# Kernel tuning notes

Measured on AMD Instinct MI355X. Metric: run time of the kernel, lower is better.

## Reference

```python
import jax, jax.numpy as jnp
import numpy as np

B, T, D, DO = 8, 2048, 1024, 1024

def setup_inputs() -> dict:
    key = jax.random.key(0)
    ks = jax.random.split(key, 7)
    s = 1.0 / np.sqrt(D)
    return {
        "input_tensor": jax.random.normal(ks[0], (B, T, D), dtype=jnp.float32),
        "Wq": jax.random.uniform(ks[1], (D, D), jnp.float32, -s, s),
        "bq": jax.random.uniform(ks[2], (D,), jnp.float32, -s, s),
        "Wk": jax.random.uniform(ks[3], (D, D), jnp.float32, -s, s),
        "bk": jax.random.uniform(ks[4], (D,), jnp.float32, -s, s),
        "Wv": jax.random.uniform(ks[5], (D, DO), jnp.float32, -s, s),
        "bv": jax.random.uniform(ks[6], (DO,), jnp.float32, -s, s),
    }

def reference(input_tensor, Wq, bq, Wk, bk, Wv, bv):
    scale = jnp.sqrt(jnp.float32(input_tensor.shape[-1]))
    q = input_tensor @ Wq + bq            # [B,T,D]
    k = input_tensor @ Wk + bk            # [B,T,D]
    v = input_tensor @ Wv + bv            # [B,T,DO]
    scores = jnp.einsum('btd,bsd->bts', q, k) / scale  # [B,T,T]
    attn = jax.nn.softmax(scores, axis=-1)
    return jnp.einsum('bts,bso->bto', attn, v)         # [B,T,DO]
```

## Files before the change

kernel.cpp:

```cpp
#include <hip/hip_runtime.h>
#include <stdint.h>

typedef unsigned short u16;
typedef __attribute__((ext_vector_type(4))) float    floatx4;
typedef __attribute__((ext_vector_type(8))) __bf16   bf16x8;
typedef __attribute__((ext_vector_type(2))) unsigned int uintx2;
typedef __attribute__((ext_vector_type(4))) unsigned int uintx4;

__device__ inline u16 f2bf(float f) {
  unsigned int u = __builtin_bit_cast(unsigned int, f);
  u += 0x7fffu + ((u >> 16) & 1u);
  return (u16)(u >> 16);
}

#define GLD16(gsrc, ldst)                                                        \
  __builtin_amdgcn_global_load_lds(                                              \
      (__attribute__((address_space(1))) void*)(gsrc),                           \
      (__attribute__((address_space(3))) void*)(ldst), 16, 0, 0)

#define SB() __builtin_amdgcn_sched_barrier(0)

__global__ __launch_bounds__(256) void prep_kernel(const float* __restrict__ x,
                                                   const float* __restrict__ Wq,
                                                   const float* __restrict__ Wk,
                                                   const float* __restrict__ Wv,
                                                   u16* __restrict__ xb,
                                                   u16* __restrict__ WT) {
  const int z = blockIdx.z;
  const int tid = threadIdx.y * 32 + threadIdx.x;
  if (z >= 3) {
    long blk = (long)(z - 3) * 1024 + blockIdx.y * 32 + blockIdx.x;
    long i = (blk * 256 + tid) * 8;
    floatx4 a = *(const floatx4*)(x + i);
    floatx4 b = *(const floatx4*)(x + i + 4);
    uintx4 o;
    o[0] = (unsigned)f2bf(a[0]) | ((unsigned)f2bf(a[1]) << 16);
    o[1] = (unsigned)f2bf(a[2]) | ((unsigned)f2bf(a[3]) << 16);
    o[2] = (unsigned)f2bf(b[0]) | ((unsigned)f2bf(b[1]) << 16);
    o[3] = (unsigned)f2bf(b[2]) | ((unsigned)f2bf(b[3]) << 16);
    *(uintx4*)(xb + i) = o;
    return;
  }
  __shared__ float tile[32][33];
  const float* W = (z == 0) ? Wq : (z == 1) ? Wk : Wv;
  u16* dst = WT + (long)z * 1024 * 1024;
  int bx = blockIdx.x * 32, by = blockIdx.y * 32;
  int tx = threadIdx.x, ty = threadIdx.y;
  for (int i = 0; i < 32; i += 8)
    tile[ty + i][tx] = W[(long)(by + ty + i) * 1024 + bx + tx];
  __syncthreads();
  for (int i = 0; i < 32; i += 8)
    dst[(long)(bx + ty + i) * 1024 + by + tx] = f2bf(tile[tx][ty + i]);
}

#define BM 256
#define BN 256
#define BK 64

template <int MODE, int GN>
__global__ __launch_bounds__(512, 2)
void gemm_bt(const u16* __restrict__ Aall, const u16* __restrict__ Ball,
             void* __restrict__ Call, void* __restrict__ C2,
             const float* __restrict__ bias, const float* __restrict__ bias2,
             float* __restrict__ lsum,
             int M, int N, int K, long aStride, long bStride, long cStride) {
  __shared__ __align__(16) u16 As[2][BM * BK];
  __shared__ __align__(16) u16 Bs[2][BN * BK];

  const int z = blockIdx.z;
  const u16* A  = Aall + (long)z * aStride;
  const u16* Bt = Ball + (long)z * bStride;

  int m_idx, n_idx;
  {
    const int tiles_n = gridDim.x, tiles_m = gridDim.y;
    int nwg = tiles_n * tiles_m;
    int bid = blockIdx.y * tiles_n + blockIdx.x;
    int qq = nwg >> 3;
    int L = (bid & 7) * qq + (bid >> 3);
    int per_group = GN * tiles_m;
    int g = L / per_group;
    int rem = L - g * per_group;
    n_idx = g * GN + rem % GN;
    m_idx = rem / GN;
  }

  const int tid  = threadIdx.x;
  const int m0   = m_idx * BM;
  const int n0   = n_idx * BN;
  const int wave = tid >> 6;
  const int lane = tid & 63;
  const int wm   = (wave >> 2) * 128;
  const int wn   = (wave & 3) * 64;
  const int l15  = lane & 15;
  const int quad = lane >> 4;

  floatx4 acc[8][4];
  floatx4 zero = {0.f, 0.f, 0.f, 0.f};
#pragma unroll
  for (int i = 0; i < 8; ++i)
#pragma unroll
    for (int j = 0; j < 4; ++j) acc[i][j] = zero;

  const int swz   = (quad ^ (l15 & 7)) * 8;
  const int aOff0 = (wm + l15) * 64 + swz;
  const int bOff0 = (wn + l15) * 64 + swz;

  const u16* gA[4];
  const u16* gB[4];
#pragma unroll
  for (int i = 0; i < 4; ++i) {
    int ci = i * 512 + tid;
    int r = ci >> 3, sc = ci & 7;
    int col = (sc ^ (r & 7)) * 8;
    gA[i] = A  + (long)(m0 + r) * K + col;
    gB[i] = Bt + (long)(n0 + r) * K + col;
  }

  const int nt = K / BK;

  {
    u16* lA = (u16*)As + tid * 8;
    u16* lB = (u16*)Bs + tid * 8;
    GLD16(gB[0], lB);          GLD16(gB[1], lB + 4096);
    GLD16(gB[2], lB + 8192);   GLD16(gB[3], lB + 12288);
    GLD16(gA[0], lA);          GLD16(gA[2], lA + 8192);
    GLD16(gA[1], lA + 4096);   GLD16(gA[3], lA + 12288);
  }
  SB();
  asm volatile("s_waitcnt vmcnt(0)" ::: "memory");
  SB();
  __builtin_amdgcn_s_barrier();
  SB();
#pragma unroll
  for (int i = 0; i < 4; ++i) { gA[i] += BK; gB[i] += BK; }

  for (int t = 0; t < nt; ++t) {
    const int cur = t & 1;
    const int bo  = cur << 14;
    const u16* aP0 = (const u16*)As + bo + aOff0;
    const u16* bP0 = (const u16*)Bs + bo + bOff0;
    const u16* aP1 = (const u16*)As + bo + (aOff0 ^ 32);
    const u16* bP1 = (const u16*)Bs + bo + (bOff0 ^ 32);
    u16* ldsAn = (u16*)As + (bo ^ 16384) + tid * 8;
    u16* ldsBn = (u16*)Bs + (bo ^ 16384) + tid * 8;
    const bool st1 = (t + 1 < nt);
    bf16x8 afA[4], afB[4], bfr[4];

#pragma unroll
    for (int mi = 0; mi < 4; ++mi)
      afA[mi] = *(const bf16x8*)(aP0 + mi * 1024);
#pragma unroll
    for (int ni = 0; ni < 4; ++ni)
      bfr[ni] = *(const bf16x8*)(bP0 + ni * 1024);
    if (st1) { GLD16(gB[0], ldsBn); GLD16(gB[1], ldsBn + 4096); }
    SB();
    if (st1) asm volatile("s_waitcnt vmcnt(2)" ::: "memory");
    else     asm volatile("s_waitcnt vmcnt(0)" ::: "memory");
    SB();
    __builtin_amdgcn_s_barrier();
    asm volatile("s_waitcnt lgkmcnt(0)" ::: "memory");
    SB();
    __builtin_amdgcn_s_setprio(1);
#pragma unroll
    for (int mi = 0; mi < 4; ++mi)
#pragma unroll
      for (int ni = 0; ni < 4; ++ni)
        acc[mi][ni] = __builtin_amdgcn_mfma_f32_16x16x32_bf16(
            bfr[ni], afA[mi], acc[mi][ni], 0, 0, 0);
    __builtin_amdgcn_s_setprio(0);
    SB();

#pragma unroll
    for (int mi = 0; mi < 4; ++mi)
      afB[mi] = *(const bf16x8*)(aP0 + 4096 + mi * 1024);
    if (st1) { GLD16(gB[2], ldsBn + 8192); GLD16(gB[3], ldsBn + 12288); }
    SB();
    __builtin_amdgcn_s_barrier();
    asm volatile("s_waitcnt lgkmcnt(0)" ::: "memory");
    SB();
    __builtin_amdgcn_s_setprio(1);
#pragma unroll
    for (int mi = 0; mi < 4; ++mi)
#pragma unroll
      for (int ni = 0; ni < 4; ++ni)
        acc[4 + mi][ni] = __builtin_amdgcn_mfma_f32_16x16x32_bf16(
            bfr[ni], afB[mi], acc[4 + mi][ni], 0, 0, 0);
    __builtin_amdgcn_s_setprio(0);
    SB();

#pragma unroll
    for (int mi = 0; mi < 4; ++mi)
      afA[mi] = *(const bf16x8*)(aP1 + mi * 1024);
#pragma unroll
    for (int ni = 0; ni < 4; ++ni)
      bfr[ni] = *(const bf16x8*)(bP1 + ni * 1024);
    if (st1) { GLD16(gA[0], ldsAn); GLD16(gA[2], ldsAn + 8192); }
    SB();
    __builtin_amdgcn_s_barrier();
    asm volatile("s_waitcnt lgkmcnt(0)" ::: "memory");
    SB();
    __builtin_amdgcn_s_setprio(1);
#pragma unroll
    for (int mi = 0; mi < 4; ++mi)
#pragma unroll
      for (int ni = 0; ni < 4; ++ni)
        acc[mi][ni] = __builtin_amdgcn_mfma_f32_16x16x32_bf16(
            bfr[ni], afA[mi], acc[mi][ni], 0, 0, 0);
    __builtin_amdgcn_s_setprio(0);
    SB();

#pragma unroll
    for (int mi = 0; mi < 4; ++mi)
      afB[mi] = *(const bf16x8*)(aP1 + 4096 + mi * 1024);
    if (st1) { GLD16(gA[1], ldsAn + 4096); GLD16(gA[3], ldsAn + 12288); }
    SB();
    if (st1) asm volatile("s_waitcnt vmcnt(2)" ::: "memory");
    SB();
    __builtin_amdgcn_s_barrier();
    asm volatile("s_waitcnt lgkmcnt(0)" ::: "memory");
    SB();
    __builtin_amdgcn_s_setprio(1);
#pragma unroll
    for (int mi = 0; mi < 4; ++mi)
#pragma unroll
      for (int ni = 0; ni < 4; ++ni)
        acc[4 + mi][ni] = __builtin_amdgcn_mfma_f32_16x16x32_bf16(
            bfr[ni], afB[mi], acc[4 + mi][ni], 0, 0, 0);
    __builtin_amdgcn_s_setprio(0);
    SB();

#pragma unroll
    for (int i = 0; i < 4; ++i) { gA[i] += BK; gB[i] += BK; }
  }

#pragma unroll
  for (int mi = 0; mi < 8; ++mi) {
    const int row = m0 + wm + mi * 16 + l15;
    if (MODE == 2) {
      u16* C = (u16*)Call + (long)z * cStride;
      float rs = 0.f;
#pragma unroll
      for (int ni = 0; ni < 4; ++ni) {
        int colb = n0 + wn + ni * 16 + quad * 4;
        floatx4 v = acc[mi][ni];
        float e0 = __expf(v[0] * 0.03125f), e1 = __expf(v[1] * 0.03125f);
        float e2 = __expf(v[2] * 0.03125f), e3 = __expf(v[3] * 0.03125f);
        rs += (e0 + e1) + (e2 + e3);
        uintx2 o;
        o[0] = (unsigned)f2bf(e0) | ((unsigned)f2bf(e1) << 16);
        o[1] = (unsigned)f2bf(e2) | ((unsigned)f2bf(e3) << 16);
        *(uintx2*)(C + (long)row * N + colb) = o;
      }
      rs += __shfl_xor(rs, 16);
      rs += __shfl_xor(rs, 32);
      if (quad == 0) atomicAdd(lsum + (long)z * 2048 + row, rs);
    } else if (MODE == 3) {
      float* C = (float*)Call + (long)z * cStride;
      float inv = 1.0f / lsum[(long)z * 2048 + row];
#pragma unroll
      for (int ni = 0; ni < 4; ++ni) {
        int colb = n0 + wn + ni * 16 + quad * 4;
        floatx4 v = acc[mi][ni];
        floatx4 o = {v[0] * inv, v[1] * inv, v[2] * inv, v[3] * inv};
        *(floatx4*)(C + (long)row * N + colb) = o;
      }
    } else if (MODE == 0) {
#pragma unroll
      for (int ni = 0; ni < 4; ++ni) {
        int colb = n0 + wn + ni * 16 + quad * 4;
        u16* C = (colb < 1024) ? (u16*)Call : (u16*)C2;
        const float* bp = (colb < 1024) ? bias + colb : bias2 + (colb - 1024);
        floatx4 b = *(const floatx4*)bp;
        floatx4 v = acc[mi][ni];
        uintx2 o;
        o[0] = (unsigned)f2bf(v[0] + b[0]) | ((unsigned)f2bf(v[1] + b[1]) << 16);
        o[1] = (unsigned)f2bf(v[2] + b[2]) | ((unsigned)f2bf(v[3] + b[3]) << 16);
        *(uintx2*)(C + (long)row * 1024 + (colb & 1023)) = o;
      }
    } else {
      u16* C = (u16*)Call;
      float b = bias[row];
#pragma unroll
      for (int ni = 0; ni < 4; ++ni) {
        int colb = n0 + wn + ni * 16 + quad * 4;
        long base = ((long)(colb >> 11) * 1024) * 2048 + (colb & 2047);
        floatx4 v = acc[mi][ni];
        uintx2 o;
        o[0] = (unsigned)f2bf(v[0] + b) | ((unsigned)f2bf(v[1] + b) << 16);
        o[1] = (unsigned)f2bf(v[2] + b) | ((unsigned)f2bf(v[3] + b) << 16);
        *(uintx2*)(C + base + (long)row * 2048) = o;
      }
    }
  }
}

extern "C" void kernel_launch(void* const* d_in, const int* in_sizes, int n_in,
                              void* d_out, int out_size, void* d_ws, size_t ws_size,
                              hipStream_t stream) {
  const float* x  = (const float*)d_in[0];
  const float* Wq = (const float*)d_in[1];
  const float* bq = (const float*)d_in[2];
  const float* Wk = (const float*)d_in[3];
  const float* bk = (const float*)d_in[4];
  const float* Wv = (const float*)d_in[5];
  const float* bv = (const float*)d_in[6];
  float* out = (float*)d_out;

  const long BT = 16384;
  u16* xb = (u16*)d_ws;
  u16* WT = xb + BT * 1024;
  u16* qb = WT + 3L * 1024 * 1024;
  u16* kb = qb + BT * 1024;
  u16* vT = kb + BT * 1024;
  u16* S  = vT + BT * 1024;
  float* lsum = (float*)(S + 8L * 2048 * 2048);

  hipMemsetAsync(lsum, 0, 8 * 2048 * sizeof(float), stream);

  prep_kernel<<<dim3(32, 32, 11), dim3(32, 8), 0, stream>>>(x, Wq, Wk, Wv, xb, WT);

  gemm_bt<0, 8><<<dim3(8, 64, 1), 512, 0, stream>>>(
      xb, WT, qb, kb, bq, bk, nullptr, 16384, 2048, 1024, 0, 0, 0);
  gemm_bt<1, 8><<<dim3(64, 4, 1), 512, 0, stream>>>(
      WT + 2L * 1024 * 1024, xb, vT, nullptr, bv, nullptr, nullptr,
      1024, 16384, 1024, 0, 0, 0);
  gemm_bt<2, 8><<<dim3(8, 8, 8), 512, 0, stream>>>(
      qb, kb, S, nullptr, nullptr, nullptr, lsum,
      2048, 2048, 1024, 2048L * 1024, 2048L * 1024, 2048L * 2048);
  gemm_bt<3, 4><<<dim3(4, 8, 8), 512, 0, stream>>>(
      S, vT, out, nullptr, nullptr, nullptr, lsum,
      2048, 1024, 2048, 2048L * 2048, 1024L * 2048, 2048L * 1024);
}
```

Before: 392.1 us.

## Shrink GEMM tiles to 128x128 and simplify the double-buffered pipeline

Reduces the block tile from 256x256 to 128x128 and raises the occupancy hint to 4 blocks per CU. The K-loop is restructured from four interleaved sub-phases with staggered global loads to two phases, each issuing all next-tile loads at once followed by a full vmcnt(0) wait. Grids are scaled up to match. This trades per-block data reuse and overlap for more blocks and better load balance across CUs, at the risk of more memory traffic and less latency hiding.

```diff
diff --git a/kernel.cpp b/kernel.cpp
--- a/kernel.cpp
+++ b/kernel.cpp
@@ -53,12 +53,12 @@
     dst[(long)(bx + ty + i) * 1024 + by + tx] = f2bf(tile[tx][ty + i]);
 }
 
-#define BM 256
-#define BN 256
+#define BM 128
+#define BN 128
 #define BK 64
 
 template <int MODE, int GN>
-__global__ __launch_bounds__(512, 2)
+__global__ __launch_bounds__(512, 4)
 void gemm_bt(const u16* __restrict__ Aall, const u16* __restrict__ Ball,
              void* __restrict__ Call, void* __restrict__ C2,
              const float* __restrict__ bias, const float* __restrict__ bias2,
@@ -90,26 +90,26 @@
   const int n0   = n_idx * BN;
   const int wave = tid >> 6;
   const int lane = tid & 63;
-  const int wm   = (wave >> 2) * 128;
-  const int wn   = (wave & 3) * 64;
+  const int wm   = (wave >> 2) * 64;
+  const int wn   = (wave & 3) * 32;
   const int l15  = lane & 15;
   const int quad = lane >> 4;
 
-  floatx4 acc[8][4];
+  floatx4 acc[4][2];
   floatx4 zero = {0.f, 0.f, 0.f, 0.f};
 #pragma unroll
-  for (int i = 0; i < 8; ++i)
-#pragma unroll
-    for (int j = 0; j < 4; ++j) acc[i][j] = zero;
+  for (int i = 0; i < 4; ++i)
+#pragma unroll
+    for (int j = 0; j < 2; ++j) acc[i][j] = zero;
 
   const int swz   = (quad ^ (l15 & 7)) * 8;
   const int aOff0 = (wm + l15) * 64 + swz;
   const int bOff0 = (wn + l15) * 64 + swz;
 
-  const u16* gA[4];
-  const u16* gB[4];
-#pragma unroll
-  for (int i = 0; i < 4; ++i) {
+  const u16* gA[2];
+  const u16* gB[2];
+#pragma unroll
+  for (int i = 0; i < 2; ++i) {
     int ci = i * 512 + tid;
     int r = ci >> 3, sc = ci & 7;
     int col = (sc ^ (r & 7)) * 8;
@@ -122,10 +122,8 @@
   {
     u16* lA = (u16*)As + tid * 8;
     u16* lB = (u16*)Bs + tid * 8;
-    GLD16(gB[0], lB);          GLD16(gB[1], lB + 4096);
-    GLD16(gB[2], lB + 8192);   GLD16(gB[3], lB + 12288);
-    GLD16(gA[0], lA);          GLD16(gA[2], lA + 8192);
-    GLD16(gA[1], lA + 4096);   GLD16(gA[3], lA + 12288);
+    GLD16(gA[0], lA); GLD16(gA[1], lA + 4096);
+    GLD16(gB[0], lB); GLD16(gB[1], lB + 4096);
   }
   SB();
   asm volatile("s_waitcnt vmcnt(0)" ::: "memory");
@@ -133,30 +131,30 @@
   __builtin_amdgcn_s_barrier();
   SB();
 #pragma unroll
-  for (int i = 0; i < 4; ++i) { gA[i] += BK; gB[i] += BK; }
+  for (int i = 0; i < 2; ++i) { gA[i] += BK; gB[i] += BK; }
 
   for (int t = 0; t < nt; ++t) {
     const int cur = t & 1;
-    const int bo  = cur << 14;
+    const int bo  = cur << 13;
     const u16* aP0 = (const u16*)As + bo + aOff0;
     const u16* bP0 = (const u16*)Bs + bo + bOff0;
     const u16* aP1 = (const u16*)As + bo + (aOff0 ^ 32);
     const u16* bP1 = (const u16*)Bs + bo + (bOff0 ^ 32);
-    u16* ldsAn = (u16*)As + (bo ^ 16384) + tid * 8;
-    u16* ldsBn = (u16*)Bs + (bo ^ 16384) + tid * 8;
+    u16* ldsAn = (u16*)As + (bo ^ 8192) + tid * 8;
+    u16* ldsBn = (u16*)Bs + (bo ^ 8192) + tid * 8;
     const bool st1 = (t + 1 < nt);
-    bf16x8 afA[4], afB[4], bfr[4];
-
-#pragma unroll
-    for (int mi = 0; mi < 4; ++mi)
-      afA[mi] = *(const bf16x8*)(aP0 + mi * 1024);
-#pragma unroll
-    for (int ni = 0; ni < 4; ++ni)
+    bf16x8 af[4], bfr[2];
+
+#pragma unroll
+    for (int mi = 0; mi < 4; ++mi)
+      af[mi] = *(const bf16x8*)(aP0 + mi * 1024);
+#pragma unroll
+    for (int ni = 0; ni < 2; ++ni)
       bfr[ni] = *(const bf16x8*)(bP0 + ni * 1024);
-    if (st1) { GLD16(gB[0], ldsBn); GLD16(gB[1], ldsBn + 4096); }
-    SB();
-    if (st1) asm volatile("s_waitcnt vmcnt(2)" ::: "memory");
-    else     asm volatile("s_waitcnt vmcnt(0)" ::: "memory");
+    if (st1) {
+      GLD16(gA[0], ldsAn); GLD16(gA[1], ldsAn + 4096);
+      GLD16(gB[0], ldsBn); GLD16(gB[1], ldsBn + 4096);
+    }
     SB();
     __builtin_amdgcn_s_barrier();
     asm volatile("s_waitcnt lgkmcnt(0)" ::: "memory");
@@ -165,16 +163,20 @@
 #pragma unroll
     for (int mi = 0; mi < 4; ++mi)
 #pragma unroll
-      for (int ni = 0; ni < 4; ++ni)
+      for (int ni = 0; ni < 2; ++ni)
         acc[mi][ni] = __builtin_amdgcn_mfma_f32_16x16x32_bf16(
-            bfr[ni], afA[mi], acc[mi][ni], 0, 0, 0);
+            bfr[ni], af[mi], acc[mi][ni], 0, 0, 0);
     __builtin_amdgcn_s_setprio(0);
     SB();
 
 #pragma unroll
     for (int mi = 0; mi < 4; ++mi)
-      afB[mi] = *(const bf16x8*)(aP0 + 4096 + mi * 1024);
-    if (st1) { GLD16(gB[2], ldsBn + 8192); GLD16(gB[3], ldsBn + 12288); }
+      af[mi] = *(const bf16x8*)(aP1 + mi * 1024);
+#pragma unroll
+    for (int ni = 0; ni < 2; ++ni)
+      bfr[ni] = *(const bf16x8*)(bP1 + ni * 1024);
+    SB();
+    asm volatile("s_waitcnt vmcnt(0)" ::: "memory");
     SB();
     __builtin_amdgcn_s_barrier();
     asm volatile("s_waitcnt lgkmcnt(0)" ::: "memory");
@@ -183,65 +185,24 @@
 #pragma unroll
     for (int mi = 0; mi < 4; ++mi)
 #pragma unroll
-      for (int ni = 0; ni < 4; ++ni)
-        acc[4 + mi][ni] = __builtin_amdgcn_mfma_f32_16x16x32_bf16(
-            bfr[ni], afB[mi], acc[4 + mi][ni], 0, 0, 0);
+      for (int ni = 0; ni < 2; ++ni)
+        acc[mi][ni] = __builtin_amdgcn_mfma_f32_16x16x32_bf16(
+            bfr[ni], af[mi], acc[mi][ni], 0, 0, 0);
     __builtin_amdgcn_s_setprio(0);
     SB();
 
 #pragma unroll
-    for (int mi = 0; mi < 4; ++mi)
-      afA[mi] = *(const bf16x8*)(aP1 + mi * 1024);
-#pragma unroll
-    for (int ni = 0; ni < 4; ++ni)
-      bfr[ni] = *(const bf16x8*)(bP1 + ni * 1024);
-    if (st1) { GLD16(gA[0], ldsAn); GLD16(gA[2], ldsAn + 8192); }
-    SB();
-    __builtin_amdgcn_s_barrier();
-    asm volatile("s_waitcnt lgkmcnt(0)" ::: "memory");
-    SB();
-    __builtin_amdgcn_s_setprio(1);
-#pragma unroll
-    for (int mi = 0; mi < 4; ++mi)
-#pragma unroll
-      for (int ni = 0; ni < 4; ++ni)
-        acc[mi][ni] = __builtin_amdgcn_mfma_f32_16x16x32_bf16(
-            bfr[ni], afA[mi], acc[mi][ni], 0, 0, 0);
-    __builtin_amdgcn_s_setprio(0);
-    SB();
-
-#pragma unroll
-    for (int mi = 0; mi < 4; ++mi)
-      afB[mi] = *(const bf16x8*)(aP1 + 4096 + mi * 1024);
-    if (st1) { GLD16(gA[1], ldsAn + 4096); GLD16(gA[3], ldsAn + 12288); }
-    SB();
-    if (st1) asm volatile("s_waitcnt vmcnt(2)" ::: "memory");
-    SB();
-    __builtin_amdgcn_s_barrier();
-    asm volatile("s_waitcnt lgkmcnt(0)" ::: "memory");
-    SB();
-    __builtin_amdgcn_s_setprio(1);
-#pragma unroll
-    for (int mi = 0; mi < 4; ++mi)
-#pragma unroll
-      for (int ni = 0; ni < 4; ++ni)
-        acc[4 + mi][ni] = __builtin_amdgcn_mfma_f32_16x16x32_bf16(
-            bfr[ni], afB[mi], acc[4 + mi][ni], 0, 0, 0);
-    __builtin_amdgcn_s_setprio(0);
-    SB();
-
-#pragma unroll
-    for (int i = 0; i < 4; ++i) { gA[i] += BK; gB[i] += BK; }
-  }
-
-#pragma unroll
-  for (int mi = 0; mi < 8; ++mi) {
+    for (int i = 0; i < 2; ++i) { gA[i] += BK; gB[i] += BK; }
+  }
+
+#pragma unroll
+  for (int mi = 0; mi < 4; ++mi) {
     const int row = m0 + wm + mi * 16 + l15;
     if (MODE == 2) {
       u16* C = (u16*)Call + (long)z * cStride;
       float rs = 0.f;
 #pragma unroll
-      for (int ni = 0; ni < 4; ++ni) {
+      for (int ni = 0; ni < 2; ++ni) {
         int colb = n0 + wn + ni * 16 + quad * 4;
         floatx4 v = acc[mi][ni];
         float e0 = __expf(v[0] * 0.03125f), e1 = __expf(v[1] * 0.03125f);
@@ -259,7 +220,7 @@
       float* C = (float*)Call + (long)z * cStride;
       float inv = 1.0f / lsum[(long)z * 2048 + row];
 #pragma unroll
-      for (int ni = 0; ni < 4; ++ni) {
+      for (int ni = 0; ni < 2; ++ni) {
         int colb = n0 + wn + ni * 16 + quad * 4;
         floatx4 v = acc[mi][ni];
         floatx4 o = {v[0] * inv, v[1] * inv, v[2] * inv, v[3] * inv};
@@ -267,7 +228,7 @@
       }
     } else if (MODE == 0) {
 #pragma unroll
-      for (int ni = 0; ni < 4; ++ni) {
+      for (int ni = 0; ni < 2; ++ni) {
         int colb = n0 + wn + ni * 16 + quad * 4;
         u16* C = (colb < 1024) ? (u16*)Call : (u16*)C2;
         const float* bp = (colb < 1024) ? bias + colb : bias2 + (colb - 1024);
@@ -282,7 +243,7 @@
       u16* C = (u16*)Call;
       float b = bias[row];
 #pragma unroll
-      for (int ni = 0; ni < 4; ++ni) {
+      for (int ni = 0; ni < 2; ++ni) {
         int colb = n0 + wn + ni * 16 + quad * 4;
         long base = ((long)(colb >> 11) * 1024) * 2048 + (colb & 2047);
         floatx4 v = acc[mi][ni];
@@ -320,15 +281,15 @@
 
   prep_kernel<<<dim3(32, 32, 11), dim3(32, 8), 0, stream>>>(x, Wq, Wk, Wv, xb, WT);
 
-  gemm_bt<0, 8><<<dim3(8, 64, 1), 512, 0, stream>>>(
+  gemm_bt<0, 8><<<dim3(16, 128, 1), 512, 0, stream>>>(
       xb, WT, qb, kb, bq, bk, nullptr, 16384, 2048, 1024, 0, 0, 0);
-  gemm_bt<1, 8><<<dim3(64, 4, 1), 512, 0, stream>>>(
+  gemm_bt<1, 8><<<dim3(128, 8, 1), 512, 0, stream>>>(
       WT + 2L * 1024 * 1024, xb, vT, nullptr, bv, nullptr, nullptr,
       1024, 16384, 1024, 0, 0, 0);
-  gemm_bt<2, 8><<<dim3(8, 8, 8), 512, 0, stream>>>(
+  gemm_bt<2, 8><<<dim3(16, 16, 8), 512, 0, stream>>>(
       qb, kb, S, nullptr, nullptr, nullptr, lsum,
       2048, 2048, 1024, 2048L * 1024, 2048L * 1024, 2048L * 2048);
-  gemm_bt<3, 4><<<dim3(4, 8, 8), 512, 0, stream>>>(
+  gemm_bt<3, 4><<<dim3(8, 16, 8), 512, 0, stream>>>(
       S, vT, out, nullptr, nullptr, nullptr, lsum,
       2048, 1024, 2048, 2048L * 2048, 1024L * 2048, 2048L * 1024);
 }
```

New measurement: 424.3 us. 8.2% more time.

## Restructure GEMM main loop into four M-quarter phases covering both K halves

Applied to the files above, without the earlier changes.

Reorganizes the per-tile MFMA schedule so B fragments for both K halves are loaded once up front. Each of four phases then loads two A fragments per K half and runs 16 MFMAs on a quarter of the M accumulators. The global-to-LDS prefetch issue and the vmcnt waits are redistributed across the four phases, and extra barriers are added after each phase. The aim is to shorten per-phase LDS read latency and spread the async copies more evenly, at the cost of more barriers and more live B registers.

```diff
diff --git a/kernel.cpp b/kernel.cpp
--- a/kernel.cpp
+++ b/kernel.cpp
@@ -124,8 +124,8 @@
     u16* lB = (u16*)Bs + tid * 8;
     GLD16(gB[0], lB);          GLD16(gB[1], lB + 4096);
     GLD16(gB[2], lB + 8192);   GLD16(gB[3], lB + 12288);
-    GLD16(gA[0], lA);          GLD16(gA[2], lA + 8192);
-    GLD16(gA[1], lA + 4096);   GLD16(gA[3], lA + 12288);
+    GLD16(gA[0], lA);          GLD16(gA[1], lA + 4096);
+    GLD16(gA[2], lA + 8192);   GLD16(gA[3], lA + 12288);
   }
   SB();
   asm volatile("s_waitcnt vmcnt(0)" ::: "memory");
@@ -145,89 +145,131 @@
     u16* ldsAn = (u16*)As + (bo ^ 16384) + tid * 8;
     u16* ldsBn = (u16*)Bs + (bo ^ 16384) + tid * 8;
     const bool st1 = (t + 1 < nt);
-    bf16x8 afA[4], afB[4], bfr[4];
-
-#pragma unroll
-    for (int mi = 0; mi < 4; ++mi)
-      afA[mi] = *(const bf16x8*)(aP0 + mi * 1024);
-#pragma unroll
-    for (int ni = 0; ni < 4; ++ni)
-      bfr[ni] = *(const bf16x8*)(bP0 + ni * 1024);
+    bf16x8 bfr0[4], bfr1[4];
+    bf16x8 af0[2], af1[2];
+
+#pragma unroll
+    for (int j = 0; j < 2; ++j) {
+      af0[j] = *(const bf16x8*)(aP0 + j * 1024);
+      af1[j] = *(const bf16x8*)(aP1 + j * 1024);
+    }
+#pragma unroll
+    for (int ni = 0; ni < 4; ++ni) {
+      bfr0[ni] = *(const bf16x8*)(bP0 + ni * 1024);
+      bfr1[ni] = *(const bf16x8*)(bP1 + ni * 1024);
+    }
     if (st1) { GLD16(gB[0], ldsBn); GLD16(gB[1], ldsBn + 4096); }
     SB();
+    asm volatile("s_waitcnt lgkmcnt(8)" ::: "memory");
+    SB();
+    __builtin_amdgcn_s_barrier();
+    asm volatile("s_waitcnt lgkmcnt(0)" ::: "memory");
+    SB();
+    __builtin_amdgcn_s_setprio(1);
+#pragma unroll
+    for (int j = 0; j < 2; ++j)
+#pragma unroll
+      for (int ni = 0; ni < 4; ++ni)
+        acc[j][ni] = __builtin_amdgcn_mfma_f32_16x16x32_bf16(
+            bfr0[ni], af0[j], acc[j][ni], 0, 0, 0);
+#pragma unroll
+    for (int j = 0; j < 2; ++j)
+#pragma unroll
+      for (int ni = 0; ni < 4; ++ni)
+        acc[j][ni] = __builtin_amdgcn_mfma_f32_16x16x32_bf16(
+            bfr1[ni], af1[j], acc[j][ni], 0, 0, 0);
+    __builtin_amdgcn_s_setprio(0);
+    SB();
+    __builtin_amdgcn_s_barrier();
+    SB();
+
+#pragma unroll
+    for (int j = 0; j < 2; ++j) {
+      af0[j] = *(const bf16x8*)(aP0 + (2 + j) * 1024);
+      af1[j] = *(const bf16x8*)(aP1 + (2 + j) * 1024);
+    }
+    if (st1) { GLD16(gB[2], ldsBn + 8192); GLD16(gB[3], ldsBn + 12288); }
+    SB();
+    if (st1) asm volatile("s_waitcnt vmcnt(4)" ::: "memory");
+    else     asm volatile("s_waitcnt vmcnt(0)" ::: "memory");
+    SB();
+    __builtin_amdgcn_s_barrier();
+    asm volatile("s_waitcnt lgkmcnt(0)" ::: "memory");
+    SB();
+    __builtin_amdgcn_s_setprio(1);
+#pragma unroll
+    for (int j = 0; j < 2; ++j)
+#pragma unroll
+      for (int ni = 0; ni < 4; ++ni)
+        acc[2 + j][ni] = __builtin_amdgcn_mfma_f32_16x16x32_bf16(
+            bfr0[ni], af0[j], acc[2 + j][ni], 0, 0, 0);
+#pragma unroll
+    for (int j = 0; j < 2; ++j)
+#pragma unroll
+      for (int ni = 0; ni < 4; ++ni)
+        acc[2 + j][ni] = __builtin_amdgcn_mfma_f32_16x16x32_bf16(
+            bfr1[ni], af1[j], acc[2 + j][ni], 0, 0, 0);
+    __builtin_amdgcn_s_setprio(0);
+    SB();
+    __builtin_amdgcn_s_barrier();
+    SB();
+
+#pragma unroll
+    for (int j = 0; j < 2; ++j) {
+      af0[j] = *(const bf16x8*)(aP0 + (4 + j) * 1024);
+      af1[j] = *(const bf16x8*)(aP1 + (4 + j) * 1024);
+    }
+    if (st1) { GLD16(gA[0], ldsAn); GLD16(gA[1], ldsAn + 4096); }
+    SB();
+    __builtin_amdgcn_s_barrier();
+    asm volatile("s_waitcnt lgkmcnt(0)" ::: "memory");
+    SB();
+    __builtin_amdgcn_s_setprio(1);
+#pragma unroll
+    for (int j = 0; j < 2; ++j)
+#pragma unroll
+      for (int ni = 0; ni < 4; ++ni)
+        acc[4 + j][ni] = __builtin_amdgcn_mfma_f32_16x16x32_bf16(
+            bfr0[ni], af0[j], acc[4 + j][ni], 0, 0, 0);
+#pragma unroll
+    for (int j = 0; j < 2; ++j)
+#pragma unroll
+      for (int ni = 0; ni < 4; ++ni)
+        acc[4 + j][ni] = __builtin_amdgcn_mfma_f32_16x16x32_bf16(
+            bfr1[ni], af1[j], acc[4 + j][ni], 0, 0, 0);
+    __builtin_amdgcn_s_setprio(0);
+    SB();
+    __builtin_amdgcn_s_barrier();
+    SB();
+
+#pragma unroll
+    for (int j = 0; j < 2; ++j) {
+      af0[j] = *(const bf16x8*)(aP0 + (6 + j) * 1024);
+      af1[j] = *(const bf16x8*)(aP1 + (6 + j) * 1024);
+    }
+    if (st1) { GLD16(gA[2], ldsAn + 8192); GLD16(gA[3], ldsAn + 12288); }
+    SB();
     if (st1) asm volatile("s_waitcnt vmcnt(2)" ::: "memory");
-    else     asm volatile("s_waitcnt vmcnt(0)" ::: "memory");
     SB();
     __builtin_amdgcn_s_barrier();
     asm volatile("s_waitcnt lgkmcnt(0)" ::: "memory");
     SB();
     __builtin_amdgcn_s_setprio(1);
 #pragma unroll
-    for (int mi = 0; mi < 4; ++mi)
-#pragma unroll
-      for (int ni = 0; ni < 4; ++ni)
-        acc[mi][ni] = __builtin_amdgcn_mfma_f32_16x16x32_bf16(
-            bfr[ni], afA[mi], acc[mi][ni], 0, 0, 0);
+    for (int j = 0; j < 2; ++j)
+#pragma unroll
+      for (int ni = 0; ni < 4; ++ni)
+        acc[6 + j][ni] = __builtin_amdgcn_mfma_f32_16x16x32_bf16(
+            bfr0[ni], af0[j], acc[6 + j][ni], 0, 0, 0);
+#pragma unroll
+    for (int j = 0; j < 2; ++j)
+#pragma unroll
+      for (int ni = 0; ni < 4; ++ni)
+        acc[6 + j][ni] = __builtin_amdgcn_mfma_f32_16x16x32_bf16(
+            bfr1[ni], af1[j], acc[6 + j][ni], 0, 0, 0);
     __builtin_amdgcn_s_setprio(0);
     SB();
-
-#pragma unroll
-    for (int mi = 0; mi < 4; ++mi)
-      afB[mi] = *(const bf16x8*)(aP0 + 4096 + mi * 1024);
-    if (st1) { GLD16(gB[2], ldsBn + 8192); GLD16(gB[3], ldsBn + 12288); }
-    SB();
-    __builtin_amdgcn_s_barrier();
-    asm volatile("s_waitcnt lgkmcnt(0)" ::: "memory");
-    SB();
-    __builtin_amdgcn_s_setprio(1);
-#pragma unroll
-    for (int mi = 0; mi < 4; ++mi)
-#pragma unroll
-      for (int ni = 0; ni < 4; ++ni)
-        acc[4 + mi][ni] = __builtin_amdgcn_mfma_f32_16x16x32_bf16(
-            bfr[ni], afB[mi], acc[4 + mi][ni], 0, 0, 0);
-    __builtin_amdgcn_s_setprio(0);
-    SB();
-
-#pragma unroll
-    for (int mi = 0; mi < 4; ++mi)
-      afA[mi] = *(const bf16x8*)(aP1 + mi * 1024);
-#pragma unroll
-    for (int ni = 0; ni < 4; ++ni)
-      bfr[ni] = *(const bf16x8*)(bP1 + ni * 1024);
-    if (st1) { GLD16(gA[0], ldsAn); GLD16(gA[2], ldsAn + 8192); }
-    SB();
-    __builtin_amdgcn_s_barrier();
-    asm volatile("s_waitcnt lgkmcnt(0)" ::: "memory");
-    SB();
-    __builtin_amdgcn_s_setprio(1);
-#pragma unroll
-    for (int mi = 0; mi < 4; ++mi)
-#pragma unroll
-      for (int ni = 0; ni < 4; ++ni)
-        acc[mi][ni] = __builtin_amdgcn_mfma_f32_16x16x32_bf16(
-            bfr[ni], afA[mi], acc[mi][ni], 0, 0, 0);
-    __builtin_amdgcn_s_setprio(0);
-    SB();
-
-#pragma unroll
-    for (int mi = 0; mi < 4; ++mi)
-      afB[mi] = *(const bf16x8*)(aP1 + 4096 + mi * 1024);
-    if (st1) { GLD16(gA[1], ldsAn + 4096); GLD16(gA[3], ldsAn + 12288); }
-    SB();
-    if (st1) asm volatile("s_waitcnt vmcnt(2)" ::: "memory");
-    SB();
-    __builtin_amdgcn_s_barrier();
-    asm volatile("s_waitcnt lgkmcnt(0)" ::: "memory");
-    SB();
-    __builtin_amdgcn_s_setprio(1);
-#pragma unroll
-    for (int mi = 0; mi < 4; ++mi)
-#pragma unroll
-      for (int ni = 0; ni < 4; ++ni)
-        acc[4 + mi][ni] = __builtin_amdgcn_mfma_f32_16x16x32_bf16(
-            bfr[ni], afB[mi], acc[4 + mi][ni], 0, 0, 0);
-    __builtin_amdgcn_s_setprio(0);
+    __builtin_amdgcn_s_barrier();
     SB();
 
 #pragma unroll
```

Result: slower. 400.5 us (+2.1%).

## Switch GEMM inner loop from 16x16x32 to 32x32x16 bf16 MFMA tiles

Applied to the files above, without the earlier changes.

Replaces the 16x16x32 MFMA instructions with 32x32x16 MFMAs across all GEMM modes. Each wave's 128x64 tile now uses 4x2 32x32 accumulators instead of 8x4 16x16 ones. LDS fragment loads, swizzle offsets and every epilogue's row/column mapping are rewritten to match the new accumulator layout. The aim is fewer MFMA issues and fewer LDS fragment reads per unit of work, at the risk of a different LDS bank-conflict pattern and different register pressure.

```diff
diff --git a/kernel.cpp b/kernel.cpp
--- a/kernel.cpp
+++ b/kernel.cpp
@@ -3,6 +3,7 @@
 
 typedef unsigned short u16;
 typedef __attribute__((ext_vector_type(4))) float    floatx4;
+typedef __attribute__((ext_vector_type(16))) float   floatx16;
 typedef __attribute__((ext_vector_type(8))) __bf16   bf16x8;
 typedef __attribute__((ext_vector_type(2))) unsigned int uintx2;
 typedef __attribute__((ext_vector_type(4))) unsigned int uintx4;
@@ -92,19 +93,24 @@
   const int lane = tid & 63;
   const int wm   = (wave >> 2) * 128;
   const int wn   = (wave & 3) * 64;
-  const int l15  = lane & 15;
-  const int quad = lane >> 4;
-
-  floatx4 acc[8][4];
-  floatx4 zero = {0.f, 0.f, 0.f, 0.f};
-#pragma unroll
-  for (int i = 0; i < 8; ++i)
-#pragma unroll
-    for (int j = 0; j < 4; ++j) acc[i][j] = zero;
-
-  const int swz   = (quad ^ (l15 & 7)) * 8;
-  const int aOff0 = (wm + l15) * 64 + swz;
-  const int bOff0 = (wn + l15) * 64 + swz;
+  const int l31  = lane & 31;
+  const int half = lane >> 5;
+  const int l7   = lane & 7;
+
+  floatx16 acc[4][2];
+#pragma unroll
+  for (int i = 0; i < 4; ++i)
+#pragma unroll
+    for (int j = 0; j < 2; ++j)
+#pragma unroll
+      for (int e = 0; e < 16; ++e) acc[i][j][e] = 0.f;
+
+  const int swz  = (half ^ l7) * 8;
+  const int aRow = (wm + l31) * 64;
+  const int bRow = (wn + l31) * 64;
+  int sx[4];
+#pragma unroll
+  for (int ks = 0; ks < 4; ++ks) sx[ks] = swz ^ (ks << 4);
 
   const u16* gA[4];
   const u16* gB[4];
@@ -124,8 +130,8 @@
     u16* lB = (u16*)Bs + tid * 8;
     GLD16(gB[0], lB);          GLD16(gB[1], lB + 4096);
     GLD16(gB[2], lB + 8192);   GLD16(gB[3], lB + 12288);
-    GLD16(gA[0], lA);          GLD16(gA[2], lA + 8192);
-    GLD16(gA[1], lA + 4096);   GLD16(gA[3], lA + 12288);
+    GLD16(gA[0], lA);          GLD16(gA[1], lA + 4096);
+    GLD16(gA[2], lA + 8192);   GLD16(gA[3], lA + 12288);
   }
   SB();
   asm volatile("s_waitcnt vmcnt(0)" ::: "memory");
@@ -136,23 +142,24 @@
   for (int i = 0; i < 4; ++i) { gA[i] += BK; gB[i] += BK; }
 
   for (int t = 0; t < nt; ++t) {
-    const int cur = t & 1;
-    const int bo  = cur << 14;
-    const u16* aP0 = (const u16*)As + bo + aOff0;
-    const u16* bP0 = (const u16*)Bs + bo + bOff0;
-    const u16* aP1 = (const u16*)As + bo + (aOff0 ^ 32);
-    const u16* bP1 = (const u16*)Bs + bo + (bOff0 ^ 32);
+    const int bo  = (t & 1) << 14;
+    const u16* Ap = (const u16*)As + bo + aRow;
+    const u16* Bp = (const u16*)Bs + bo + bRow;
     u16* ldsAn = (u16*)As + (bo ^ 16384) + tid * 8;
     u16* ldsBn = (u16*)Bs + (bo ^ 16384) + tid * 8;
     const bool st1 = (t + 1 < nt);
-    bf16x8 afA[4], afB[4], bfr[4];
-
-#pragma unroll
-    for (int mi = 0; mi < 4; ++mi)
-      afA[mi] = *(const bf16x8*)(aP0 + mi * 1024);
-#pragma unroll
-    for (int ni = 0; ni < 4; ++ni)
-      bfr[ni] = *(const bf16x8*)(bP0 + ni * 1024);
+    bf16x8 af[2][2], bfr[2][2];
+
+#pragma unroll
+    for (int mi = 0; mi < 2; ++mi)
+#pragma unroll
+      for (int ks = 0; ks < 2; ++ks)
+        af[mi][ks] = *(const bf16x8*)(Ap + mi * 2048 + sx[ks]);
+#pragma unroll
+    for (int ni = 0; ni < 2; ++ni)
+#pragma unroll
+      for (int ks = 0; ks < 2; ++ks)
+        bfr[ni][ks] = *(const bf16x8*)(Bp + ni * 2048 + sx[ks]);
     if (st1) { GLD16(gB[0], ldsBn); GLD16(gB[1], ldsBn + 4096); }
     SB();
     if (st1) asm volatile("s_waitcnt vmcnt(2)" ::: "memory");
@@ -163,17 +170,21 @@
     SB();
     __builtin_amdgcn_s_setprio(1);
 #pragma unroll
-    for (int mi = 0; mi < 4; ++mi)
-#pragma unroll
-      for (int ni = 0; ni < 4; ++ni)
-        acc[mi][ni] = __builtin_amdgcn_mfma_f32_16x16x32_bf16(
-            bfr[ni], afA[mi], acc[mi][ni], 0, 0, 0);
+    for (int ks = 0; ks < 2; ++ks)
+#pragma unroll
+      for (int mi = 0; mi < 2; ++mi)
+#pragma unroll
+        for (int ni = 0; ni < 2; ++ni)
+          acc[mi][ni] = __builtin_amdgcn_mfma_f32_32x32x16_bf16(
+              bfr[ni][ks], af[mi][ks], acc[mi][ni], 0, 0, 0);
     __builtin_amdgcn_s_setprio(0);
     SB();
 
 #pragma unroll
-    for (int mi = 0; mi < 4; ++mi)
-      afB[mi] = *(const bf16x8*)(aP0 + 4096 + mi * 1024);
+    for (int mi = 0; mi < 2; ++mi)
+#pragma unroll
+      for (int ks = 0; ks < 2; ++ks)
+        af[mi][ks] = *(const bf16x8*)(Ap + (2 + mi) * 2048 + sx[ks]);
     if (st1) { GLD16(gB[2], ldsBn + 8192); GLD16(gB[3], ldsBn + 12288); }
     SB();
     __builtin_amdgcn_s_barrier();
@@ -181,20 +192,26 @@
     SB();
     __builtin_amdgcn_s_setprio(1);
 #pragma unroll
-    for (int mi = 0; mi < 4; ++mi)
-#pragma unroll
-      for (int ni = 0; ni < 4; ++ni)
-        acc[4 + mi][ni] = __builtin_amdgcn_mfma_f32_16x16x32_bf16(
-            bfr[ni], afB[mi], acc[4 + mi][ni], 0, 0, 0);
+    for (int ks = 0; ks < 2; ++ks)
+#pragma unroll
+      for (int mi = 0; mi < 2; ++mi)
+#pragma unroll
+        for (int ni = 0; ni < 2; ++ni)
+          acc[2 + mi][ni] = __builtin_amdgcn_mfma_f32_32x32x16_bf16(
+              bfr[ni][ks], af[mi][ks], acc[2 + mi][ni], 0, 0, 0);
     __builtin_amdgcn_s_setprio(0);
     SB();
 
 #pragma unroll
-    for (int mi = 0; mi < 4; ++mi)
-      afA[mi] = *(const bf16x8*)(aP1 + mi * 1024);
-#pragma unroll
-    for (int ni = 0; ni < 4; ++ni)
-      bfr[ni] = *(const bf16x8*)(bP1 + ni * 1024);
+    for (int mi = 0; mi < 2; ++mi)
+#pragma unroll
+      for (int ks = 0; ks < 2; ++ks)
+        af[mi][ks] = *(const bf16x8*)(Ap + mi * 2048 + sx[2 + ks]);
+#pragma unroll
+    for (int ni = 0; ni < 2; ++ni)
+#pragma unroll
+      for (int ks = 0; ks < 2; ++ks)
+        bfr[ni][ks] = *(const bf16x8*)(Bp + ni * 2048 + sx[2 + ks]);
     if (st1) { GLD16(gA[0], ldsAn); GLD16(gA[2], ldsAn + 8192); }
     SB();
     __builtin_amdgcn_s_barrier();
@@ -202,17 +219,21 @@
     SB();
     __builtin_amdgcn_s_setprio(1);
 #pragma unroll
-    for (int mi = 0; mi < 4; ++mi)
-#pragma unroll
-      for (int ni = 0; ni < 4; ++ni)
-        acc[mi][ni] = __builtin_amdgcn_mfma_f32_16x16x32_bf16(
-            bfr[ni], afA[mi], acc[mi][ni], 0, 0, 0);
+    for (int ks = 0; ks < 2; ++ks)
+#pragma unroll
+      for (int mi = 0; mi < 2; ++mi)
+#pragma unroll
+        for (int ni = 0; ni < 2; ++ni)
+          acc[mi][ni] = __builtin_amdgcn_mfma_f32_32x32x16_bf16(
+              bfr[ni][ks], af[mi][ks], acc[mi][ni], 0, 0, 0);
     __builtin_amdgcn_s_setprio(0);
     SB();
 
 #pragma unroll
-    for (int mi = 0; mi < 4; ++mi)
-      afB[mi] = *(const bf16x8*)(aP1 + 4096 + mi * 1024);
+    for (int mi = 0; mi < 2; ++mi)
+#pragma unroll
+      for (int ks = 0; ks < 2; ++ks)
+        af[mi][ks] = *(const bf16x8*)(Ap + (2 + mi) * 2048 + sx[2 + ks]);
     if (st1) { GLD16(gA[1], ldsAn + 4096); GLD16(gA[3], ldsAn + 12288); }
     SB();
     if (st1) asm volatile("s_waitcnt vmcnt(2)" ::: "memory");
@@ -222,11 +243,13 @@
     SB();
     __builtin_amdgcn_s_setprio(1);
 #pragma unroll
-    for (int mi = 0; mi < 4; ++mi)
-#pragma unroll
-      for (int ni = 0; ni < 4; ++ni)
-        acc[4 + mi][ni] = __builtin_amdgcn_mfma_f32_16x16x32_bf16(
-            bfr[ni], afB[mi], acc[4 + mi][ni], 0, 0, 0);
+    for (int ks = 0; ks < 2; ++ks)
+#pragma unroll
+      for (int mi = 0; mi < 2; ++mi)
+#pragma unroll
+        for (int ni = 0; ni < 2; ++ni)
+          acc[2 + mi][ni] = __builtin_amdgcn_mfma_f32_32x32x16_bf16(
+              bfr[ni][ks], af[mi][ks], acc[2 + mi][ni], 0, 0, 0);
     __builtin_amdgcn_s_setprio(0);
     SB();
 
@@ -235,62 +258,74 @@
   }
 
 #pragma unroll
-  for (int mi = 0; mi < 8; ++mi) {
-    const int row = m0 + wm + mi * 16 + l15;
+  for (int mi = 0; mi < 4; ++mi) {
+    const int row = m0 + wm + mi * 32 + l31;
     if (MODE == 2) {
       u16* C = (u16*)Call + (long)z * cStride;
       float rs = 0.f;
 #pragma unroll
-      for (int ni = 0; ni < 4; ++ni) {
-        int colb = n0 + wn + ni * 16 + quad * 4;
-        floatx4 v = acc[mi][ni];
-        float e0 = __expf(v[0] * 0.03125f), e1 = __expf(v[1] * 0.03125f);
-        float e2 = __expf(v[2] * 0.03125f), e3 = __expf(v[3] * 0.03125f);
-        rs += (e0 + e1) + (e2 + e3);
-        uintx2 o;
-        o[0] = (unsigned)f2bf(e0) | ((unsigned)f2bf(e1) << 16);
-        o[1] = (unsigned)f2bf(e2) | ((unsigned)f2bf(e3) << 16);
-        *(uintx2*)(C + (long)row * N + colb) = o;
-      }
-      rs += __shfl_xor(rs, 16);
+      for (int ni = 0; ni < 2; ++ni)
+#pragma unroll
+        for (int rg = 0; rg < 4; ++rg) {
+          int colb = n0 + wn + ni * 32 + rg * 8 + half * 4;
+          float e0 = __expf(acc[mi][ni][rg * 4 + 0] * 0.03125f);
+          float e1 = __expf(acc[mi][ni][rg * 4 + 1] * 0.03125f);
+          float e2 = __expf(acc[mi][ni][rg * 4 + 2] * 0.03125f);
+          float e3 = __expf(acc[mi][ni][rg * 4 + 3] * 0.03125f);
+          rs += (e0 + e1) + (e2 + e3);
+          uintx2 o;
+          o[0] = (unsigned)f2bf(e0) | ((unsigned)f2bf(e1) << 16);
+          o[1] = (unsigned)f2bf(e2) | ((unsigned)f2bf(e3) << 16);
+          *(uintx2*)(C + (long)row * N + colb) = o;
+        }
       rs += __shfl_xor(rs, 32);
-      if (quad == 0) atomicAdd(lsum + (long)z * 2048 + row, rs);
+      if (half == 0) atomicAdd(lsum + (long)z * 2048 + row, rs);
     } else if (MODE == 3) {
       float* C = (float*)Call + (long)z * cStride;
       float inv = 1.0f / lsum[(long)z * 2048 + row];
 #pragma unroll
-      for (int ni = 0; ni < 4; ++ni) {
-        int colb = n0 + wn + ni * 16 + quad * 4;
-        floatx4 v = acc[mi][ni];
-        floatx4 o = {v[0] * inv, v[1] * inv, v[2] * inv, v[3] * inv};
-        *(floatx4*)(C + (long)row * N + colb) = o;
-      }
+      for (int ni = 0; ni < 2; ++ni)
+#pragma unroll
+        for (int rg = 0; rg < 4; ++rg) {
+          int colb = n0 + wn + ni * 32 + rg * 8 + half * 4;
+          floatx4 o = {acc[mi][ni][rg * 4 + 0] * inv,
+                       acc[mi][ni][rg * 4 + 1] * inv,
+                       acc[mi][ni][rg * 4 + 2] * inv,
+                       acc[mi][ni][rg * 4 + 3] * inv};
+          *(floatx4*)(C + (long)row * N + colb) = o;
+        }
     } else if (MODE == 0) {
 #pragma unroll
-      for (int ni = 0; ni < 4; ++ni) {
-        int colb = n0 + wn + ni * 16 + quad * 4;
-        u16* C = (colb < 1024) ? (u16*)Call : (u16*)C2;
-        const float* bp = (colb < 1024) ? bias + colb : bias2 + (colb - 1024);
-        floatx4 b = *(const floatx4*)bp;
-        floatx4 v = acc[mi][ni];
-        uintx2 o;
-        o[0] = (unsigned)f2bf(v[0] + b[0]) | ((unsigned)f2bf(v[1] + b[1]) << 16);
-        o[1] = (unsigned)f2bf(v[2] + b[2]) | ((unsigned)f2bf(v[3] + b[3]) << 16);
-        *(uintx2*)(C + (long)row * 1024 + (colb & 1023)) = o;
-      }
+      for (int ni = 0; ni < 2; ++ni)
+#pragma unroll
+        for (int rg = 0; rg < 4; ++rg) {
+          int colb = n0 + wn + ni * 32 + rg * 8 + half * 4;
+          u16* C = (colb < 1024) ? (u16*)Call : (u16*)C2;
+          const float* bp = (colb < 1024) ? bias + colb : bias2 + (colb - 1024);
+          floatx4 b = *(const floatx4*)bp;
+          uintx2 o;
+          o[0] = (unsigned)f2bf(acc[mi][ni][rg * 4 + 0] + b[0]) |
+                 ((unsigned)f2bf(acc[mi][ni][rg * 4 + 1] + b[1]) << 16);
+          o[1] = (unsigned)f2bf(acc[mi][ni][rg * 4 + 2] + b[2]) |
+                 ((unsigned)f2bf(acc[mi][ni][rg * 4 + 3] + b[3]) << 16);
+          *(uintx2*)(C + (long)row * 1024 + (colb & 1023)) = o;
+        }
     } else {
       u16* C = (u16*)Call;
       float b = bias[row];
 #pragma unroll
-      for (int ni = 0; ni < 4; ++ni) {
-        int colb = n0 + wn + ni * 16 + quad * 4;
-        long base = ((long)(colb >> 11) * 1024) * 2048 + (colb & 2047);
-        floatx4 v = acc[mi][ni];
-        uintx2 o;
-        o[0] = (unsigned)f2bf(v[0] + b) | ((unsigned)f2bf(v[1] + b) << 16);
-        o[1] = (unsigned)f2bf(v[2] + b) | ((unsigned)f2bf(v[3] + b) << 16);
-        *(uintx2*)(C + base + (long)row * 2048) = o;
-      }
+      for (int ni = 0; ni < 2; ++ni)
+#pragma unroll
+        for (int rg = 0; rg < 4; ++rg) {
+          int colb = n0 + wn + ni * 32 + rg * 8 + half * 4;
+          long base = ((long)(colb >> 11) * 1024) * 2048 + (colb & 2047);
+          uintx2 o;
+          o[0] = (unsigned)f2bf(acc[mi][ni][rg * 4 + 0] + b) |
+                 ((unsigned)f2bf(acc[mi][ni][rg * 4 + 1] + b) << 16);
+          o[1] = (unsigned)f2bf(acc[mi][ni][rg * 4 + 2] + b) |
+                 ((unsigned)f2bf(acc[mi][ni][rg * 4 + 3] + b) << 16);
+          *(uintx2*)(C + base + (long)row * 2048) = o;
+        }
     }
   }
 }
```

New measurement: 403.2 us. 2.8% more time.
